# Kernel tuning notes

Measured on AMD Instinct MI355X. Metric: run time of the kernel, lower is better.

The kernel has to match this reference:

```python
import jax, jax.numpy as jnp
import numpy as np

N_NODES = 100000
N_EDGES = 500000
D_IN = 128
D_HID = 256
D_OUT = 1


def mish(x):
    # x * tanh(softplus(x))
    return x * jnp.tanh(jax.nn.softplus(x))


def setup_inputs() -> dict:
    key = jax.random.key(0)
    k1, k2, k3, k4, k5, k6 = jax.random.split(key, 6)
    z = jax.random.normal(k1, (N_NODES, D_IN), dtype=jnp.float32)
    edge = jax.random.randint(k2, (2, N_EDGES), 0, N_NODES, dtype=jnp.int64)
    # PyTorch Linear default init: U(-1/sqrt(fan_in), 1/sqrt(fan_in))
    s1 = 1.0 / np.sqrt(D_IN)
    s2 = 1.0 / np.sqrt(D_HID)
    W1 = jax.random.uniform(k3, (D_HID, D_IN), minval=-s1, maxval=s1, dtype=jnp.float32)
    b1 = jax.random.uniform(k4, (D_HID,), minval=-s1, maxval=s1, dtype=jnp.float32)
    W2 = jax.random.uniform(k5, (D_OUT, D_HID), minval=-s2, maxval=s2, dtype=jnp.float32)
    b2 = jax.random.uniform(k6, (D_OUT,), minval=-s2, maxval=s2, dtype=jnp.float32)
    return {"z": z, "edge": edge, "W1": W1, "b1": b1, "W2": W2, "b2": b2}


def reference(z, edge, W1, b1, W2, b2):
    # gather node pairs and elementwise product: [E, D_IN]
    x = z[edge[0]] * z[edge[1]]
    # fc1 + mish (dropout is identity in eval mode)
    h = mish(jnp.einsum('ed,hd->eh', x, W1) + b1)
    # fc2 + sigmoid -> [E, 1]
    logits = jnp.einsum('eh,oh->eo', h, W2) + b2
    return jax.nn.sigmoid(logits)
```

## Files before the change

kernel.cpp:

```cpp
#include <hip/hip_runtime.h>
#include <hip/hip_bf16.h>
#include <hip/hip_fp16.h>
#include <type_traits>


#define N_NODES 100000
#define N_EDGES 500000
#define D_IN    128
#define D_HID   256
#define PAIRS   (N_EDGES / 32)
#define GRID    512
#define NWAVES  16
#define TOTAL_WAVES (GRID * NWAVES)
#define LDS_ROW 288

#define LOG2E 1.44269504f
#define LN2   0.69314718f

typedef _Float16 half8  __attribute__((ext_vector_type(8)));
typedef __fp16   fp16x2 __attribute__((ext_vector_type(2)));
typedef __bf16   bf16x8 __attribute__((ext_vector_type(8)));
typedef float    f32x4  __attribute__((ext_vector_type(4)));

__device__ __forceinline__ unsigned int pkh_u32(float a, float b) {
    fp16x2 r = __builtin_amdgcn_cvt_pkrtz(a, b);
    return __builtin_bit_cast(unsigned int, r);
}
__device__ __forceinline__ unsigned int pkbf_u32(float a, float b) {
    union { __hip_bfloat162 v; unsigned int u; } c;
    c.v = __float22bfloat162_rn(make_float2(a, b));
    return c.u;
}
__device__ __forceinline__ float exp2a(float x) {
    float r; asm("v_exp_f32 %0, %1" : "=v"(r) : "v"(x)); return r;
}
__device__ __forceinline__ float sigf(float x) {
    return __builtin_amdgcn_rcpf(1.0f + __expf(-x));
}

__global__ __launch_bounds__(256)
void zcvt_kernel(const float* __restrict__ z, _Float16* __restrict__ zh) {
    const size_t i = (size_t)blockIdx.x * 256 + threadIdx.x;
    const float4 f0 = *reinterpret_cast<const float4*>(z + i * 8);
    const float4 f1 = *reinterpret_cast<const float4*>(z + i * 8 + 4);
    union { half8 h; uint4 u; } o;
    o.h[0] = (_Float16)f0.x; o.h[1] = (_Float16)f0.y;
    o.h[2] = (_Float16)f0.z; o.h[3] = (_Float16)f0.w;
    o.h[4] = (_Float16)f1.x; o.h[5] = (_Float16)f1.y;
    o.h[6] = (_Float16)f1.z; o.h[7] = (_Float16)f1.w;
    *reinterpret_cast<uint4*>(zh + i * 8) = o.u;
}

template <bool USE_H>
__global__ __launch_bounds__(1024, 8)
void edge_mlp_kernel(const float*    __restrict__ z,
                     const _Float16* __restrict__ zh,
                     const int*      __restrict__ edge,
                     const float*    __restrict__ W1,
                     const float*    __restrict__ b1,
                     const float*    __restrict__ W2,
                     const float*    __restrict__ b2,
                     float*          __restrict__ out) {
    using frag_t = std::conditional_t<USE_H, half8, bf16x8>;

    __shared__ __align__(16) char smem[2048 + D_HID * LDS_ROW];

    const int t = threadIdx.x;

    if (t < 256) {
        ((float*)smem)[t]          = b1[t] * LOG2E;
        ((float*)(smem + 1024))[t] = W2[t] * LN2;
    }
    #pragma unroll
    for (int i = 0; i < 4; ++i) {
        const int c    = t + i * 1024;
        const int h    = c >> 4;
        const int slot = c & 15;
        const float* src = W1 + h * D_IN + slot * 8;
        const float4 f0 = *reinterpret_cast<const float4*>(src);
        const float4 f1 = *reinterpret_cast<const float4*>(src + 4);
        uint4 o;
        if constexpr (USE_H) {
            o = make_uint4(pkh_u32(f0.x * LOG2E, f0.y * LOG2E),
                           pkh_u32(f0.z * LOG2E, f0.w * LOG2E),
                           pkh_u32(f1.x * LOG2E, f1.y * LOG2E),
                           pkh_u32(f1.z * LOG2E, f1.w * LOG2E));
        } else {
            o = make_uint4(pkbf_u32(f0.x * LOG2E, f0.y * LOG2E),
                           pkbf_u32(f0.z * LOG2E, f0.w * LOG2E),
                           pkbf_u32(f1.x * LOG2E, f1.y * LOG2E),
                           pkbf_u32(f1.z * LOG2E, f1.w * LOG2E));
        }
        *reinterpret_cast<uint4*>(smem + 2048 + h * LDS_ROW + slot * 16) = o;
    }
    __syncthreads();

    const int wave = t >> 6;
    const int lane = t & 63;
    const int quad = lane >> 4;
    const int nlo  = lane & 15;
    const int gw   = (blockIdx.x << 4) + wave;

    const char*  ldsA  = smem + 2048 + nlo * LDS_ROW + quad * 16;
    const float* ldsB1 = (const float*)(smem + quad * 16);
    const float* ldsW2 = (const float*)(smem + 1024 + quad * 16);
    const float  b2f   = b2[0];
    const int    qoffH = quad * 16;
    const int    qoffF = quad * 32;

    for (int pi = gw; pi < PAIRS; pi += TOTAL_WAVES) {
        const int e0 = pi * 32 + nlo;
        const int u0 = edge[e0],      v0 = edge[N_EDGES + e0];
        const int u1 = edge[e0 + 16], v1 = edge[N_EDGES + e0 + 16];

        frag_t bf0[4], bf1[4];
        if constexpr (USE_H) {
            const char* zb = reinterpret_cast<const char*>(zh);
            const int ou0 = (u0 << 8) + qoffH, ov0 = (v0 << 8) + qoffH;
            const int ou1 = (u1 << 8) + qoffH, ov1 = (v1 << 8) + qoffH;
            #pragma unroll
            for (int ks = 0; ks < 4; ++ks) {
                bf0[ks] = *reinterpret_cast<const half8*>(zb + ou0 + ks * 64) *
                          *reinterpret_cast<const half8*>(zb + ov0 + ks * 64);
                bf1[ks] = *reinterpret_cast<const half8*>(zb + ou1 + ks * 64) *
                          *reinterpret_cast<const half8*>(zb + ov1 + ks * 64);
            }
        } else {
            const char* zb = reinterpret_cast<const char*>(z) + qoffF;
            const char* pu0 = zb + ((size_t)u0 << 9);
            const char* pv0 = zb + ((size_t)v0 << 9);
            const char* pu1 = zb + ((size_t)u1 << 9);
            const char* pv1 = zb + ((size_t)v1 << 9);
            #pragma unroll
            for (int ks = 0; ks < 4; ++ks) {
                float4 a0 = *reinterpret_cast<const float4*>(pu0 + ks * 128);
                float4 a1 = *reinterpret_cast<const float4*>(pu0 + ks * 128 + 16);
                float4 c0 = *reinterpret_cast<const float4*>(pv0 + ks * 128);
                float4 c1 = *reinterpret_cast<const float4*>(pv0 + ks * 128 + 16);
                union { uint4 u; bf16x8 v; } o;
                o.u = make_uint4(pkbf_u32(a0.x*c0.x*LOG2E, a0.y*c0.y*LOG2E),
                                 pkbf_u32(a0.z*c0.z*LOG2E, a0.w*c0.w*LOG2E),
                                 pkbf_u32(a1.x*c1.x*LOG2E, a1.y*c1.y*LOG2E),
                                 pkbf_u32(a1.z*c1.z*LOG2E, a1.w*c1.w*LOG2E));
                bf0[ks] = o.v;
            }
            #pragma unroll
            for (int ks = 0; ks < 4; ++ks) {
                float4 a0 = *reinterpret_cast<const float4*>(pu1 + ks * 128);
                float4 a1 = *reinterpret_cast<const float4*>(pu1 + ks * 128 + 16);
                float4 c0 = *reinterpret_cast<const float4*>(pv1 + ks * 128);
                float4 c1 = *reinterpret_cast<const float4*>(pv1 + ks * 128 + 16);
                union { uint4 u; bf16x8 v; } o;
                o.u = make_uint4(pkbf_u32(a0.x*c0.x*LOG2E, a0.y*c0.y*LOG2E),
                                 pkbf_u32(a0.z*c0.z*LOG2E, a0.w*c0.w*LOG2E),
                                 pkbf_u32(a1.x*c1.x*LOG2E, a1.y*c1.y*LOG2E),
                                 pkbf_u32(a1.z*c1.z*LOG2E, a1.w*c1.w*LOG2E));
                bf1[ks] = o.v;
            }
        }

        float l0 = 0.0f, l1 = 0.0f;
        #pragma unroll 2
        for (int g = 0; g < 16; ++g) {
            const float4 b1v = *reinterpret_cast<const float4*>(ldsB1 + g * 16);
            f32x4 acc0 = (f32x4){b1v.x, b1v.y, b1v.z, b1v.w};
            f32x4 acc1 = acc0;
            const char* lA = ldsA + g * (16 * LDS_ROW);
            #pragma unroll
            for (int ks = 0; ks < 4; ++ks) {
                frag_t wf = *reinterpret_cast<const frag_t*>(lA + ks * 64);
                if constexpr (USE_H) {
                    acc0 = __builtin_amdgcn_mfma_f32_16x16x32_f16(wf, bf0[ks], acc0, 0, 0, 0);
                    acc1 = __builtin_amdgcn_mfma_f32_16x16x32_f16(wf, bf1[ks], acc1, 0, 0, 0);
                } else {
                    acc0 = __builtin_amdgcn_mfma_f32_16x16x32_bf16(wf, bf0[ks], acc0, 0, 0, 0);
                    acc1 = __builtin_amdgcn_mfma_f32_16x16x32_bf16(wf, bf1[ks], acc1, 0, 0, 0);
                }
            }
            const float4 w2v = *reinterpret_cast<const float4*>(ldsW2 + g * 16);
            const float ww[4] = {w2v.x, w2v.y, w2v.z, w2v.w};
            #pragma unroll
            for (int i = 0; i < 4; ++i) {
                {
                    float xs = acc0[i];
                    float E  = exp2a(fminf(xs, 28.854f));
                    float num = E * (E + 2.0f);
                    l0 = fmaf(xs * num * __builtin_amdgcn_rcpf(num + 2.0f), ww[i], l0);
                }
                {
                    float xs = acc1[i];
                    float E  = exp2a(fminf(xs, 28.854f));
                    float num = E * (E + 2.0f);
                    l1 = fmaf(xs * num * __builtin_amdgcn_rcpf(num + 2.0f), ww[i], l1);
                }
            }
        }

        l0 += __shfl_xor(l0, 16);  l0 += __shfl_xor(l0, 32);
        l1 += __shfl_xor(l1, 16);  l1 += __shfl_xor(l1, 32);
        if (quad == 0) {
            out[pi * 32 + nlo]      = sigf(l0 + b2f);
            out[pi * 32 + 16 + nlo] = sigf(l1 + b2f);
        }
    }
}

extern "C" void kernel_launch(void* const* d_in, const int* in_sizes, int n_in,
                              void* d_out, int out_size, void* d_ws, size_t ws_size,
                              hipStream_t stream) {
    const float* z    = (const float*)d_in[0];
    const int*   edge = (const int*)d_in[1];
    const float* W1   = (const float*)d_in[2];
    const float* b1   = (const float*)d_in[3];
    const float* W2   = (const float*)d_in[4];
    const float* b2   = (const float*)d_in[5];
    float* out = (float*)d_out;

    const size_t zh_bytes = (size_t)N_NODES * D_IN * sizeof(_Float16);
    if (d_ws != nullptr && ws_size >= zh_bytes) {
        _Float16* zh = (_Float16*)d_ws;
        zcvt_kernel<<<dim3(N_NODES * D_IN / 8 / 256), dim3(256), 0, stream>>>(z, zh);
        edge_mlp_kernel<true><<<dim3(GRID), dim3(1024), 0, stream>>>(
            z, zh, edge, W1, b1, W2, b2, out);
    } else {
        edge_mlp_kernel<false><<<dim3(GRID), dim3(1024), 0, stream>>>(
            z, nullptr, edge, W1, b1, W2, b2, out);
    }
}
```

Measured before the change: 165.0 us.

## Drop fp16 z pre-conversion pass and gather fp32 rows directly with bf16 MFMA

Removes the separate kernel that converted z to fp16 in workspace. The edge kernel now always gathers fp32 node rows, multiplies them and packs the products to bf16 for MFMA. Blocks shrink from 1024 to 512 threads, with 8 waves per block and the grid size unchanged, so half as many waves are launched in total. It also stops scaling the activations by LOG2E on the bf16 path, which previously double-applied the scale together with the pre-scaled W1. The trade is skipping a full pass over z against twice the gather bytes per edge and less latency hiding.

New measurement: 169.9 us. 1.03x slower.

```diff
diff --git a/kernel.cpp b/kernel.cpp
--- a/kernel.cpp
+++ b/kernel.cpp
@@ -1,7 +1,6 @@
 #include <hip/hip_runtime.h>
 #include <hip/hip_bf16.h>
 #include <hip/hip_fp16.h>
-#include <type_traits>
 
 
 #define N_NODES 100000
@@ -10,22 +9,16 @@
 #define D_HID   256
 #define PAIRS   (N_EDGES / 32)
 #define GRID    512
-#define NWAVES  16
+#define NWAVES  8
 #define TOTAL_WAVES (GRID * NWAVES)
 #define LDS_ROW 288
 
 #define LOG2E 1.44269504f
 #define LN2   0.69314718f
 
-typedef _Float16 half8  __attribute__((ext_vector_type(8)));
-typedef __fp16   fp16x2 __attribute__((ext_vector_type(2)));
-typedef __bf16   bf16x8 __attribute__((ext_vector_type(8)));
-typedef float    f32x4  __attribute__((ext_vector_type(4)));
+typedef __bf16 bf16x8 __attribute__((ext_vector_type(8)));
+typedef float  f32x4  __attribute__((ext_vector_type(4)));
 
-__device__ __forceinline__ unsigned int pkh_u32(float a, float b) {
-    fp16x2 r = __builtin_amdgcn_cvt_pkrtz(a, b);
-    return __builtin_bit_cast(unsigned int, r);
-}
 __device__ __forceinline__ unsigned int pkbf_u32(float a, float b) {
     union { __hip_bfloat162 v; unsigned int u; } c;
     c.v = __float22bfloat162_rn(make_float2(a, b));
@@ -38,31 +31,14 @@
     return __builtin_amdgcn_rcpf(1.0f + __expf(-x));
 }
 
-__global__ __launch_bounds__(256)
-void zcvt_kernel(const float* __restrict__ z, _Float16* __restrict__ zh) {
-    const size_t i = (size_t)blockIdx.x * 256 + threadIdx.x;
-    const float4 f0 = *reinterpret_cast<const float4*>(z + i * 8);
-    const float4 f1 = *reinterpret_cast<const float4*>(z + i * 8 + 4);
-    union { half8 h; uint4 u; } o;
-    o.h[0] = (_Float16)f0.x; o.h[1] = (_Float16)f0.y;
-    o.h[2] = (_Float16)f0.z; o.h[3] = (_Float16)f0.w;
-    o.h[4] = (_Float16)f1.x; o.h[5] = (_Float16)f1.y;
-    o.h[6] = (_Float16)f1.z; o.h[7] = (_Float16)f1.w;
-    *reinterpret_cast<uint4*>(zh + i * 8) = o.u;
-}
-
-template <bool USE_H>
-__global__ __launch_bounds__(1024, 8)
-void edge_mlp_kernel(const float*    __restrict__ z,
-                     const _Float16* __restrict__ zh,
-                     const int*      __restrict__ edge,
-                     const float*    __restrict__ W1,
-                     const float*    __restrict__ b1,
-                     const float*    __restrict__ W2,
-                     const float*    __restrict__ b2,
-                     float*          __restrict__ out) {
-    using frag_t = std::conditional_t<USE_H, half8, bf16x8>;
-
+__global__ __launch_bounds__(512, 4)
+void edge_mlp_kernel(const float* __restrict__ z,
+                     const int*   __restrict__ edge,
+                     const float* __restrict__ W1,
+                     const float* __restrict__ b1,
+                     const float* __restrict__ W2,
+                     const float* __restrict__ b2,
+                     float*       __restrict__ out) {
     __shared__ __align__(16) char smem[2048 + D_HID * LDS_ROW];
 
     const int t = threadIdx.x;
@@ -72,25 +48,17 @@
         ((float*)(smem + 1024))[t] = W2[t] * LN2;
     }
     #pragma unroll
-    for (int i = 0; i < 4; ++i) {
-        const int c    = t + i * 1024;
+    for (int i = 0; i < 8; ++i) {
+        const int c    = t + i * 512;
         const int h    = c >> 4;
         const int slot = c & 15;
         const float* src = W1 + h * D_IN + slot * 8;
         const float4 f0 = *reinterpret_cast<const float4*>(src);
         const float4 f1 = *reinterpret_cast<const float4*>(src + 4);
-        uint4 o;
-        if constexpr (USE_H) {
-            o = make_uint4(pkh_u32(f0.x * LOG2E, f0.y * LOG2E),
-                           pkh_u32(f0.z * LOG2E, f0.w * LOG2E),
-                           pkh_u32(f1.x * LOG2E, f1.y * LOG2E),
-                           pkh_u32(f1.z * LOG2E, f1.w * LOG2E));
-        } else {
-            o = make_uint4(pkbf_u32(f0.x * LOG2E, f0.y * LOG2E),
-                           pkbf_u32(f0.z * LOG2E, f0.w * LOG2E),
-                           pkbf_u32(f1.x * LOG2E, f1.y * LOG2E),
-                           pkbf_u32(f1.z * LOG2E, f1.w * LOG2E));
-        }
+        uint4 o = make_uint4(pkbf_u32(f0.x * LOG2E, f0.y * LOG2E),
+                             pkbf_u32(f0.z * LOG2E, f0.w * LOG2E),
+                             pkbf_u32(f1.x * LOG2E, f1.y * LOG2E),
+                             pkbf_u32(f1.z * LOG2E, f1.w * LOG2E));
         *reinterpret_cast<uint4*>(smem + 2048 + h * LDS_ROW + slot * 16) = o;
     }
     __syncthreads();
@@ -99,34 +67,21 @@
     const int lane = t & 63;
     const int quad = lane >> 4;
     const int nlo  = lane & 15;
-    const int gw   = (blockIdx.x << 4) + wave;
+    const int gw   = (blockIdx.x << 3) + wave;
 
     const char*  ldsA  = smem + 2048 + nlo * LDS_ROW + quad * 16;
     const float* ldsB1 = (const float*)(smem + quad * 16);
     const float* ldsW2 = (const float*)(smem + 1024 + quad * 16);
     const float  b2f   = b2[0];
-    const int    qoffH = quad * 16;
-    const int    qoffF = quad * 32;
 
     for (int pi = gw; pi < PAIRS; pi += TOTAL_WAVES) {
         const int e0 = pi * 32 + nlo;
         const int u0 = edge[e0],      v0 = edge[N_EDGES + e0];
         const int u1 = edge[e0 + 16], v1 = edge[N_EDGES + e0 + 16];
 
-        frag_t bf0[4], bf1[4];
-        if constexpr (USE_H) {
-            const char* zb = reinterpret_cast<const char*>(zh);
-            const int ou0 = (u0 << 8) + qoffH, ov0 = (v0 << 8) + qoffH;
-            const int ou1 = (u1 << 8) + qoffH, ov1 = (v1 << 8) + qoffH;
-            #pragma unroll
-            for (int ks = 0; ks < 4; ++ks) {
-                bf0[ks] = *reinterpret_cast<const half8*>(zb + ou0 + ks * 64) *
-                          *reinterpret_cast<const half8*>(zb + ov0 + ks * 64);
-                bf1[ks] = *reinterpret_cast<const half8*>(zb + ou1 + ks * 64) *
-                          *reinterpret_cast<const half8*>(zb + ov1 + ks * 64);
-            }
-        } else {
-            const char* zb = reinterpret_cast<const char*>(z) + qoffF;
+        bf16x8 bf0[4], bf1[4];
+        {
+            const char* zb  = reinterpret_cast<const char*>(z) + quad * 32;
             const char* pu0 = zb + ((size_t)u0 << 9);
             const char* pv0 = zb + ((size_t)v0 << 9);
             const char* pu1 = zb + ((size_t)u1 << 9);
@@ -138,10 +93,10 @@
                 float4 c0 = *reinterpret_cast<const float4*>(pv0 + ks * 128);
                 float4 c1 = *reinterpret_cast<const float4*>(pv0 + ks * 128 + 16);
                 union { uint4 u; bf16x8 v; } o;
-                o.u = make_uint4(pkbf_u32(a0.x*c0.x*LOG2E, a0.y*c0.y*LOG2E),
-                                 pkbf_u32(a0.z*c0.z*LOG2E, a0.w*c0.w*LOG2E),
-                                 pkbf_u32(a1.x*c1.x*LOG2E, a1.y*c1.y*LOG2E),
-                                 pkbf_u32(a1.z*c1.z*LOG2E, a1.w*c1.w*LOG2E));
+                o.u = make_uint4(pkbf_u32(a0.x * c0.x, a0.y * c0.y),
+                                 pkbf_u32(a0.z * c0.z, a0.w * c0.w),
+                                 pkbf_u32(a1.x * c1.x, a1.y * c1.y),
+                                 pkbf_u32(a1.z * c1.z, a1.w * c1.w));
                 bf0[ks] = o.v;
             }
             #pragma unroll
@@ -151,10 +106,10 @@
                 float4 c0 = *reinterpret_cast<const float4*>(pv1 + ks * 128);
                 float4 c1 = *reinterpret_cast<const float4*>(pv1 + ks * 128 + 16);
                 union { uint4 u; bf16x8 v; } o;
-                o.u = make_uint4(pkbf_u32(a0.x*c0.x*LOG2E, a0.y*c0.y*LOG2E),
-                                 pkbf_u32(a0.z*c0.z*LOG2E, a0.w*c0.w*LOG2E),
-                                 pkbf_u32(a1.x*c1.x*LOG2E, a1.y*c1.y*LOG2E),
-                                 pkbf_u32(a1.z*c1.z*LOG2E, a1.w*c1.w*LOG2E));
+                o.u = make_uint4(pkbf_u32(a0.x * c0.x, a0.y * c0.y),
+                                 pkbf_u32(a0.z * c0.z, a0.w * c0.w),
+                                 pkbf_u32(a1.x * c1.x, a1.y * c1.y),
+                                 pkbf_u32(a1.z * c1.z, a1.w * c1.w));
                 bf1[ks] = o.v;
             }
         }
@@ -168,28 +123,23 @@
             const char* lA = ldsA + g * (16 * LDS_ROW);
             #pragma unroll
             for (int ks = 0; ks < 4; ++ks) {
-                frag_t wf = *reinterpret_cast<const frag_t*>(lA + ks * 64);
-                if constexpr (USE_H) {
-                    acc0 = __builtin_amdgcn_mfma_f32_16x16x32_f16(wf, bf0[ks], acc0, 0, 0, 0);
-                    acc1 = __builtin_amdgcn_mfma_f32_16x16x32_f16(wf, bf1[ks], acc1, 0, 0, 0);
-                } else {
-                    acc0 = __builtin_amdgcn_mfma_f32_16x16x32_bf16(wf, bf0[ks], acc0, 0, 0, 0);
-                    acc1 = __builtin_amdgcn_mfma_f32_16x16x32_bf16(wf, bf1[ks], acc1, 0, 0, 0);
-                }
+                bf16x8 wf = *reinterpret_cast<const bf16x8*>(lA + ks * 64);
+                acc0 = __builtin_amdgcn_mfma_f32_16x16x32_bf16(wf, bf0[ks], acc0, 0, 0, 0);
+                acc1 = __builtin_amdgcn_mfma_f32_16x16x32_bf16(wf, bf1[ks], acc1, 0, 0, 0);
             }
             const float4 w2v = *reinterpret_cast<const float4*>(ldsW2 + g * 16);
             const float ww[4] = {w2v.x, w2v.y, w2v.z, w2v.w};
             #pragma unroll
             for (int i = 0; i < 4; ++i) {
                 {
-                    float xs = acc0[i];
-                    float E  = exp2a(fminf(xs, 28.854f));
+                    float xs  = acc0[i];
+                    float E   = exp2a(fminf(xs, 28.854f));
                     float num = E * (E + 2.0f);
                     l0 = fmaf(xs * num * __builtin_amdgcn_rcpf(num + 2.0f), ww[i], l0);
                 }
                 {
-                    float xs = acc1[i];
-                    float E  = exp2a(fminf(xs, 28.854f));
+                    float xs  = acc1[i];
+                    float E   = exp2a(fminf(xs, 28.854f));
                     float num = E * (E + 2.0f);
                     l1 = fmaf(xs * num * __builtin_amdgcn_rcpf(num + 2.0f), ww[i], l1);
                 }
@@ -216,14 +166,6 @@
     const float* b2   = (const float*)d_in[5];
     float* out = (float*)d_out;
 
-    const size_t zh_bytes = (size_t)N_NODES * D_IN * sizeof(_Float16);
-    if (d_ws != nullptr && ws_size >= zh_bytes) {
-        _Float16* zh = (_Float16*)d_ws;
-        zcvt_kernel<<<dim3(N_NODES * D_IN / 8 / 256), dim3(256), 0, stream>>>(z, zh);
-        edge_mlp_kernel<true><<<dim3(GRID), dim3(1024), 0, stream>>>(
-            z, zh, edge, W1, b1, W2, b2, out);
-    } else {
-        edge_mlp_kernel<false><<<dim3(GRID), dim3(1024), 0, stream>>>(
-            z, nullptr, edge, W1, b1, W2, b2, out);
-    }
+    edge_mlp_kernel<<<dim3(GRID), dim3(512), 0, stream>>>(
+        z, edge, W1, b1, W2, b2, out);
 }
```
